# Performance work log

Measured on AMD Instinct MI355X. Metric: run time of the kernel, lower is better.

The kernel has to match this reference:

```python
import jax, jax.numpy as jnp
import numpy as np

N_POINTS = 400000
N_SEG = 4096


def setup_inputs() -> dict:
    key = jax.random.key(0)
    ks = jax.random.split(key, 8)
    inp = {
        "features": jax.random.normal(ks[0], (N_POINTS, 11), dtype=jnp.float32),
        "super_indices": jax.random.randint(ks[1], (N_POINTS,), 0, N_SEG, dtype=jnp.int64) if jax.config.jax_enable_x64 else jax.random.randint(ks[1], (N_POINTS,), 0, N_SEG).astype(jnp.int32),
        "num_segments": N_SEG,
        "W1": jax.random.normal(ks[2], (11, 128), dtype=jnp.float32) * 0.02,
        "b1": jnp.zeros((128,), jnp.float32),
        "W2": jax.random.normal(ks[3], (128, 256), dtype=jnp.float32) * 0.02,
        "b2": jnp.zeros((256,), jnp.float32),
        "W3": jax.random.normal(ks[4], (512, 512), dtype=jnp.float32) * 0.02,
        "b3": jnp.zeros((512,), jnp.float32),
        "W4": jax.random.normal(ks[5], (512, 384), dtype=jnp.float32) * 0.02,
        "b4": jnp.zeros((384,), jnp.float32),
    }
    return inp


def reference(features, super_indices, num_segments, W1, b1, W2, b2, W3, b3, W4, b4):
    # first_conv: two 1x1 Conv1d == per-point linears (no activation between, as in source)
    h = features @ W1 + b1            # [N,128]
    h = h @ W2 + b2                   # [N,256]
    # per-superpoint global max (torch.max over group points)
    g = jax.ops.segment_max(h, super_indices, num_segments=num_segments)  # [S,256]
    # concat broadcasted group-global with local features -> 512 channels
    hcat = jnp.concatenate([g[super_indices], h], axis=-1)                # [N,512]
    # second_conv: Conv1d(512,512,1) -> ReLU -> Conv1d(512,token_embed_dim,1)
    z = jax.nn.relu(hcat @ W3 + b3)   # [N,512]
    z = z @ W4 + b4                   # [N,384]
    # final per-superpoint max pool -> one token per superpoint
    sp_features = jax.ops.segment_max(z, super_indices, num_segments=num_segments)  # [S,384]
    return sp_features
```

## Files before the change

### kernel.cpp

```cpp
#include <hip/hip_runtime.h>
#include <stdint.h>

#define GAS __attribute__((address_space(1)))
#define LAS __attribute__((address_space(3)))

typedef unsigned short u16;
typedef short short8 __attribute__((ext_vector_type(8)));
typedef __bf16 bf16x8 __attribute__((ext_vector_type(8)));
typedef float floatx4 __attribute__((ext_vector_type(4)));

__device__ __forceinline__ u16 f2bf(float f) {
  uint32_t u = __builtin_bit_cast(uint32_t, f);
  u += 0x7FFFu + ((u >> 16) & 1u);
  return (u16)(u >> 16);
}
__device__ __forceinline__ float bf2f(u16 h) {
  return __builtin_bit_cast(float, (uint32_t)h << 16);
}
__device__ __forceinline__ void split_bf(float v, u16& hi, u16& lo) {
  hi = f2bf(v);
  float r = v - bf2f(hi);
  if (!(r == r)) r = 0.f;
  lo = f2bf(r);
}

__device__ __forceinline__ void atomicMaxF(float* addr, float val) {
  if (!(val > *(volatile const float*)addr)) return;
  if (val >= 0.f) atomicMax((int*)addr, __builtin_bit_cast(int, val));
  else            atomicMin((unsigned int*)addr, __builtin_bit_cast(unsigned int, val));
}

__device__ __forceinline__ void async16(const void* g, const void* lds) {
  __builtin_amdgcn_global_load_lds((GAS const uint32_t*)g, (LAS uint32_t*)lds, 16, 0, 0);
}

__device__ __forceinline__ floatx4 mfma_bf16(short8 a, short8 b, floatx4 c) {
  return __builtin_amdgcn_mfma_f32_16x16x32_bf16(
      __builtin_bit_cast(bf16x8, a), __builtin_bit_cast(bf16x8, b), c, 0, 0, 0);
}

__global__ void k_init(float* __restrict__ g, float* __restrict__ out,
                       int* __restrict__ hist, int ng, int no, int nh) {
  int i = blockIdx.x * 256 + threadIdx.x;
  if (i < ng) g[i] = -INFINITY;
  else if (i < ng + no) out[i - ng] = -INFINITY;
  else if (i < ng + no + nh) hist[i - ng - no] = 0;
}

__global__ void k_hist(const int* __restrict__ idx, int* __restrict__ hist, int n) {
  int p = blockIdx.x * 256 + threadIdx.x;
  if (p < n) atomicAdd(&hist[idx[p]], 1);
}

__global__ __launch_bounds__(1024) void k_scan(const int* __restrict__ hist,
                                               int* __restrict__ offs, int* __restrict__ cur) {
  __shared__ int buf[2][1024];
  int t = threadIdx.x;
  int local[4];
  int s = 0;
#pragma unroll
  for (int j = 0; j < 4; ++j) { local[j] = hist[t * 4 + j]; s += local[j]; }
  buf[0][t] = s;
  __syncthreads();
  int pb = 0;
  for (int d = 1; d < 1024; d <<= 1) {
    int v = buf[pb][t] + (t >= d ? buf[pb][t - d] : 0);
    buf[pb ^ 1][t] = v;
    pb ^= 1;
    __syncthreads();
  }
  int run = (t == 0) ? 0 : buf[pb][t - 1];
#pragma unroll
  for (int j = 0; j < 4; ++j) { offs[t * 4 + j] = run; cur[t * 4 + j] = run; run += local[j]; }
}

__global__ void k_scatter(const int* __restrict__ idx, int* __restrict__ cur,
                          int* __restrict__ perm, int* __restrict__ segp, int n) {
  int p = blockIdx.x * 256 + threadIdx.x;
  if (p >= n) return;
  int s = idx[p];
  int r = atomicAdd(&cur[s], 1);
  perm[r] = p;
  segp[r] = s;
}

__global__ void k_h1(const float* __restrict__ feat, const int* __restrict__ perm,
                     const float* __restrict__ W1, const float* __restrict__ b1,
                     u16* __restrict__ h1hi, u16* __restrict__ h1lo,
                     int pt_off, int npts_chunk) {
  int gid = blockIdx.x * 256 + threadIdx.x;
  int p = gid >> 7, c = gid & 127;
  if (p >= npts_chunk) return;
  int o = perm[pt_off + p];
  float v = b1[c];
#pragma unroll
  for (int j = 0; j < 11; ++j) v += feat[o * 11 + j] * W1[j * 128 + c];
  u16 hi, lo; split_bf(v, hi, lo);
  h1hi[gid] = hi; h1lo[gid] = lo;
}

__global__ void k_wprep(const float* __restrict__ W, u16* __restrict__ bt, int K, int N) {
  int gid = blockIdx.x * 256 + threadIdx.x;
  if (gid >= K * N) return;
  int c = gid / K, k = gid - c * K;
  float v = W[(size_t)k * N + c];
  u16 hi, lo; split_bf(v, hi, lo);
  size_t b = (size_t)c * (3 * K);
  bt[b + k] = hi; bt[b + K + k] = lo; bt[b + 2 * K + k] = hi;
}

__global__ void k_w23(const float* __restrict__ W2, const float* __restrict__ W3,
                      const float* __restrict__ b2, const float* __restrict__ b3,
                      float* __restrict__ W23, float* __restrict__ b23) {
  int gid = blockIdx.x * 256 + threadIdx.x;
  if (gid < 128 * 512) {
    int j = gid >> 9, c = gid & 511;
    float s = 0.f;
#pragma unroll 4
    for (int t = 0; t < 256; ++t) s += W2[j * 256 + t] * W3[(size_t)(256 + t) * 512 + c];
    W23[gid] = s;
  } else if (gid < 128 * 512 + 512) {
    int c = gid - 128 * 512;
    float s = b3[c];
    for (int t = 0; t < 256; ++t) s += b2[t] * W3[(size_t)(256 + t) * 512 + c];
    b23[c] = s;
  }
}

__global__ void k_prep3(const float* __restrict__ W3, const float* __restrict__ W23,
                        u16* __restrict__ bt) {
  int gid = blockIdx.x * 256 + threadIdx.x;
  if (gid >= 512 * 384) return;
  int c = gid / 384, k = gid - c * 384;
  float v = (k < 256) ? W3[(size_t)k * 512 + c] : W23[(size_t)(k - 256) * 512 + c];
  u16 hi, lo; split_bf(v, hi, lo);
  size_t b = (size_t)c * 1152;
  bt[b + k] = hi; bt[b + 384 + k] = lo; bt[b + 768 + k] = hi;
}

__global__ void k_gsplit(const float* __restrict__ g, u16* __restrict__ ghi,
                         u16* __restrict__ glo, int n) {
  int i = blockIdx.x * 256 + threadIdx.x;
  if (i >= n) return;
  u16 hi, lo; split_bf(g[i], hi, lo);
  ghi[i] = hi; glo[i] = lo;
}

template <int MODE, int KP, int NT, int CW>
__global__ __launch_bounds__(256) void k_gemm(
    const u16* __restrict__ a0, const u16* __restrict__ a1,
    const u16* __restrict__ a2, const u16* __restrict__ a3,
    const u16* __restrict__ bt, const float* __restrict__ bias,
    const int* __restrict__ segp, int mt0, int nb,
    float* __restrict__ gmax, u16* __restrict__ whi, u16* __restrict__ wlo) {
  __shared__ __align__(16) union {
    struct { u16 A[2][128 * 64]; u16 B[2][128 * 64]; } st;
    float ct[128 * 66];
  } sm;
  const int tid = threadIdx.x;
  const int w = tid >> 6, lane = tid & 63;

  const int work_total = nb * NT;
  const int spx = (work_total + 7) >> 3;
  const int wk = (blockIdx.x & 7) * spx + (blockIdx.x >> 3);
  if (wk >= work_total) return;
  const int mtl = wk / NT, ct = wk - mtl * NT;

  const int wr = w & 1, wc = w >> 1;
  const int l15 = lane & 15, l4 = lane >> 4;
  const int sub = lane >> 3;
  const int kc8 = (lane & 7) * 8;

  int arl[4], bcol[4], gq[4];
#pragma unroll
  for (int q = 0; q < 4; ++q) {
    int rr = (q * 4 + w) * 8 + sub;
    arl[q] = mtl * 128 + rr;
    bcol[q] = ct * 128 + rr;
    if constexpr (MODE == 1) gq[q] = segp[(mt0 + mtl) * 128 + rr];
  }

  auto stage = [&](int kt, int buf) {
    const int kbase = kt * 64 + kc8;
#pragma unroll
    for (int q = 0; q < 4; ++q) {
      const u16* src;
      if constexpr (MODE == 0) {
        int r = kbase >> 7, k = kbase & 127;
        src = ((r == 2) ? a1 : a0) + (size_t)arl[q] * 128 + k;
      } else if constexpr (MODE == 1) {
        int r = kbase / 384, inner = kbase - r * 384;
        bool lo = (r == 2);
        if (inner < 256) src = (lo ? a2 : a0) + (size_t)gq[q] * 256 + inner;
        else             src = (lo ? a3 : a1) + (size_t)arl[q] * 128 + (inner - 256);
      } else {
        int r = kbase >> 9, inner = kbase & 511;
        src = ((r == 2) ? a1 : a0) + (size_t)arl[q] * 512 + inner;
      }
      async16(src, &sm.st.A[buf][(q * 4 + w) * 512]);
    }
#pragma unroll
    for (int q = 0; q < 4; ++q)
      async16(bt + (size_t)bcol[q] * KP + kbase, &sm.st.B[buf][(q * 4 + w) * 512]);
  };

  floatx4 zero = {0.f, 0.f, 0.f, 0.f};
  floatx4 acc[4][4];
#pragma unroll
  for (int mi = 0; mi < 4; ++mi)
#pragma unroll
    for (int ni = 0; ni < 4; ++ni) acc[mi][ni] = zero;

  constexpr int NKT = KP / 64;
  stage(0, 0);
  __syncthreads();
  int cur = 0;
  for (int kt = 0; kt < NKT; ++kt) {
    if (kt + 1 < NKT) stage(kt + 1, cur ^ 1);
#pragma unroll
    for (int kk = 0; kk < 2; ++kk) {
      short8 af[4], bfr[4];
#pragma unroll
      for (int mi = 0; mi < 4; ++mi)
        af[mi] = *(const short8*)&sm.st.A[cur][(wr * 64 + mi * 16 + l15) * 64 + kk * 32 + l4 * 8];
#pragma unroll
      for (int ni = 0; ni < 4; ++ni)
        bfr[ni] = *(const short8*)&sm.st.B[cur][(wc * 64 + ni * 16 + l15) * 64 + kk * 32 + l4 * 8];
#pragma unroll
      for (int mi = 0; mi < 4; ++mi)
#pragma unroll
        for (int ni = 0; ni < 4; ++ni)
          acc[mi][ni] = mfma_bf16(af[mi], bfr[ni], acc[mi][ni]);
    }
    __syncthreads();
    cur ^= 1;
  }

  if constexpr (MODE == 1) {
#pragma unroll
    for (int ni = 0; ni < 4; ++ni) {
      const int col = ct * 128 + wc * 64 + ni * 16 + l15;
      const float bv = bias[col];
#pragma unroll
      for (int mi = 0; mi < 4; ++mi) {
        const int rl0 = mtl * 128 + wr * 64 + mi * 16 + l4 * 4;
#pragma unroll
        for (int r = 0; r < 4; ++r) {
          float v = fmaxf(acc[mi][ni][r] + bv, 0.f);
          u16 hi, lo; split_bf(v, hi, lo);
          whi[(size_t)(rl0 + r) * 512 + col] = hi;
          wlo[(size_t)(rl0 + r) * 512 + col] = lo;
        }
      }
    }
  } else {
#pragma unroll
    for (int h = 0; h < 2; ++h) {
      __syncthreads();
      if (wc == h) {
#pragma unroll
        for (int ni = 0; ni < 4; ++ni) {
          const int cl = ni * 16 + l15;
          const float bv = bias[ct * 128 + h * 64 + cl];
#pragma unroll
          for (int mi = 0; mi < 4; ++mi) {
            const int row0 = wr * 64 + mi * 16 + l4 * 4;
#pragma unroll
            for (int r = 0; r < 4; ++r)
              sm.ct[(row0 + r) * 66 + cl] = acc[mi][ni][r] + bv;
          }
        }
      }
      __syncthreads();
      if (tid < 128) {
        const int col = tid & 63, rh = tid >> 6;
        const int cg = ct * 128 + h * 64 + col;
        const int base = (mt0 + mtl) * 128 + rh * 64;
        float run = sm.ct[(rh * 64) * 66 + col];
        int curs = segp[base];
        for (int r = 1; r < 64; ++r) {
          int s = segp[base + r];
          float v = sm.ct[(rh * 64 + r) * 66 + col];
          if (s != curs) {
            atomicMaxF(&gmax[(size_t)curs * CW + cg], run);
            run = v; curs = s;
          } else {
            run = fmaxf(run, v);
          }
        }
        atomicMaxF(&gmax[(size_t)curs * CW + cg], run);
      }
    }
  }
}

static inline int swgrid(int work) { return 8 * ((work + 7) / 8); }

extern "C" void kernel_launch(void* const* d_in, const int* in_sizes, int n_in,
                              void* d_out, int out_size, void* d_ws, size_t ws_size,
                              hipStream_t stream) {
  const float* feat = (const float*)d_in[0];
  const int* sidx   = (const int*)d_in[1];
  const float* W1 = (const float*)d_in[3];
  const float* b1 = (const float*)d_in[4];
  const float* W2 = (const float*)d_in[5];
  const float* b2 = (const float*)d_in[6];
  const float* W3 = (const float*)d_in[7];
  const float* b3 = (const float*)d_in[8];
  const float* W4 = (const float*)d_in[9];
  const float* b4 = (const float*)d_in[10];
  float* out = (float*)d_out;
  (void)n_in;

  const int S  = out_size / 384;
  const int NP = in_sizes[1];
  const int MT = NP / 128;

  char* ws = (char*)d_ws;
  size_t off = 0;
  auto carve = [&](size_t bytes) -> void* {
    void* p = ws + off;
    off += (bytes + 255) & ~(size_t)255;
    return p;
  };
  float* g   = (float*)carve((size_t)S * 256 * 4);
  u16* ghi   = (u16*)carve((size_t)S * 256 * 2);
  u16* glo   = (u16*)carve((size_t)S * 256 * 2);
  u16* B2t   = (u16*)carve((size_t)256 * 384 * 2);
  u16* B3t   = (u16*)carve((size_t)512 * 1152 * 2);
  u16* B4t   = (u16*)carve((size_t)384 * 1536 * 2);
  float* W23 = (float*)carve((size_t)128 * 512 * 4);
  float* b23 = (float*)carve((size_t)512 * 4);
  int* hist  = (int*)carve((size_t)S * 4);
  int* offs  = (int*)carve((size_t)S * 4);
  int* curp  = (int*)carve((size_t)S * 4);
  int* perm  = (int*)carve((size_t)NP * 4);
  int* segp  = (int*)carve((size_t)NP * 4);

  const size_t per_block = (size_t)128 * (128 * 2 * 2 + 512 * 2 * 2) + 4 * 256;
  size_t remain = (ws_size > off + 4096) ? (ws_size - off - 4096) : 0;
  int cb = (int)(remain / per_block);
  if (cb < 1) cb = 1;
  if (cb > MT) cb = MT;
  u16* h1hi = (u16*)carve((size_t)cb * 128 * 128 * 2);
  u16* h1lo = (u16*)carve((size_t)cb * 128 * 128 * 2);
  u16* z1hi = (u16*)carve((size_t)cb * 128 * 512 * 2);
  u16* z1lo = (u16*)carve((size_t)cb * 128 * 512 * 2);

  k_init<<<(S * (256 + 384 + 1) + 255) / 256, 256, 0, stream>>>(g, out, hist,
                                                                S * 256, S * 384, S);
  k_hist<<<(NP + 255) / 256, 256, 0, stream>>>(sidx, hist, NP);
  k_scan<<<1, 1024, 0, stream>>>(hist, offs, curp);
  k_scatter<<<(NP + 255) / 256, 256, 0, stream>>>(sidx, curp, perm, segp, NP);

  k_wprep<<<(128 * 256 + 255) / 256, 256, 0, stream>>>(W2, B2t, 128, 256);
  k_w23<<<(128 * 512 + 512 + 255) / 256, 256, 0, stream>>>(W2, W3, b2, b3, W23, b23);
  k_prep3<<<(512 * 384 + 255) / 256, 256, 0, stream>>>(W3, W23, B3t);
  k_wprep<<<(512 * 384 + 255) / 256, 256, 0, stream>>>(W4, B4t, 512, 384);

  for (int done = 0; done < MT; done += cb) {
    int nb = (MT - done < cb) ? (MT - done) : cb;
    int pts = nb * 128;
    k_h1<<<(pts * 128) / 256, 256, 0, stream>>>(feat, perm, W1, b1, h1hi, h1lo,
                                                done * 128, pts);
    k_gemm<0, 384, 2, 256><<<swgrid(nb * 2), 256, 0, stream>>>(
        h1hi, h1lo, nullptr, nullptr, B2t, b2, segp, done, nb, g, nullptr, nullptr);
  }
  k_gsplit<<<(S * 256 + 255) / 256, 256, 0, stream>>>(g, ghi, glo, S * 256);

  for (int done = 0; done < MT; done += cb) {
    int nb = (MT - done < cb) ? (MT - done) : cb;
    int pts = nb * 128;
    k_h1<<<(pts * 128) / 256, 256, 0, stream>>>(feat, perm, W1, b1, h1hi, h1lo,
                                                done * 128, pts);
    k_gemm<1, 1152, 4, 0><<<swgrid(nb * 4), 256, 0, stream>>>(
        ghi, h1hi, glo, h1lo, B3t, b23, segp, done, nb, nullptr, z1hi, z1lo);
    k_gemm<2, 1536, 3, 384><<<swgrid(nb * 3), 256, 0, stream>>>(
        z1hi, z1lo, nullptr, nullptr, B4t, b4, segp, done, nb, out, nullptr, nullptr);
  }
}
```

Measured before the change: 2.637 ms.

## Widen GEMM N-tiles, halve K-step, and XOR-swizzle LDS staging

The GEMM kernel now takes a TILEN template parameter, so the N tile grows from 128 to 256 (or 192 for the final layer). Each block therefore reuses its staged A rows across more output columns and fewer blocks re-read the same A data. The K step drops from 64 to 32 so the shared-memory footprint stays bounded, and launch bounds ask for two blocks per CU. Staging uses an XOR chunk swizzle to avoid LDS bank conflicts, and the gathered segment indices are cached in shared memory. The cost is more accumulator registers per thread, twice as many K iterations with their barriers, and fewer blocks in flight.

```diff
diff --git a/kernel.cpp b/kernel.cpp
--- a/kernel.cpp
+++ b/kernel.cpp
@@ -146,17 +146,25 @@
   ghi[i] = hi; glo[i] = lo;
 }
 
-template <int MODE, int KP, int NT, int CW>
-__global__ __launch_bounds__(256) void k_gemm(
+template <int MODE, int KP, int NT, int CW, int TILEN>
+__global__ __launch_bounds__(256, 2) void k_gemm(
     const u16* __restrict__ a0, const u16* __restrict__ a1,
     const u16* __restrict__ a2, const u16* __restrict__ a3,
     const u16* __restrict__ bt, const float* __restrict__ bias,
     const int* __restrict__ segp, int mt0, int nb,
     float* __restrict__ gmax, u16* __restrict__ whi, u16* __restrict__ wlo) {
+  constexpr int WN = TILEN / 2;
+  constexpr int NI = WN / 16;
+  constexpr int NKT = KP / 32;
+  constexpr int NSLOT = 512 + TILEN * 4;
+  constexpr int NIT = NSLOT / 256;
+
   __shared__ __align__(16) union {
-    struct { u16 A[2][128 * 64]; u16 B[2][128 * 64]; } st;
+    struct { u16 A[2][4096]; u16 B[2][TILEN * 32]; } st;
     float ct[128 * 66];
   } sm;
+  __shared__ int segl[128];
+
   const int tid = threadIdx.x;
   const int w = tid >> 6, lane = tid & 63;
 
@@ -164,82 +172,86 @@
   const int spx = (work_total + 7) >> 3;
   const int wk = (blockIdx.x & 7) * spx + (blockIdx.x >> 3);
   if (wk >= work_total) return;
-  const int mtl = wk / NT, ct = wk - mtl * NT;
+  const int mtl = wk / NT, ctile = wk - mtl * NT;
 
   const int wr = w & 1, wc = w >> 1;
   const int l15 = lane & 15, l4 = lane >> 4;
-  const int sub = lane >> 3;
-  const int kc8 = (lane & 7) * 8;
-
-  int arl[4], bcol[4], gq[4];
-#pragma unroll
-  for (int q = 0; q < 4; ++q) {
-    int rr = (q * 4 + w) * 8 + sub;
-    arl[q] = mtl * 128 + rr;
-    bcol[q] = ct * 128 + rr;
-    if constexpr (MODE == 1) gq[q] = segp[(mt0 + mtl) * 128 + rr];
+  const int chsw = (l15 >> 1) & 3;
+
+  if constexpr (MODE == 1) {
+    if (tid < 128) segl[tid] = segp[(mt0 + mtl) * 128 + tid];
+    __syncthreads();
   }
 
   auto stage = [&](int kt, int buf) {
-    const int kbase = kt * 64 + kc8;
-#pragma unroll
-    for (int q = 0; q < 4; ++q) {
+    const int kt32 = kt * 32;
+#pragma unroll
+    for (int i = 0; i < NIT; ++i) {
+      const int s = tid + i * 256;
+      const int sw = (tid & ~63) + i * 256;
       const u16* src;
-      if constexpr (MODE == 0) {
-        int r = kbase >> 7, k = kbase & 127;
-        src = ((r == 2) ? a1 : a0) + (size_t)arl[q] * 128 + k;
-      } else if constexpr (MODE == 1) {
-        int r = kbase / 384, inner = kbase - r * 384;
-        bool lo = (r == 2);
-        if (inner < 256) src = (lo ? a2 : a0) + (size_t)gq[q] * 256 + inner;
-        else             src = (lo ? a3 : a1) + (size_t)arl[q] * 128 + (inner - 256);
+      if (s < 512) {
+        const int row = s >> 2, ch = s & 3;
+        const int kg = kt32 + ((ch ^ ((row >> 1) & 3)) << 3);
+        const int rl = mtl * 128 + row;
+        if constexpr (MODE == 0) {
+          int r = kg >> 7, k = kg & 127;
+          src = ((r == 2) ? a1 : a0) + (size_t)rl * 128 + k;
+        } else if constexpr (MODE == 1) {
+          int r = kg / 384, inner = kg - r * 384;
+          bool lo = (r == 2);
+          if (inner < 256) src = (lo ? a2 : a0) + (size_t)segl[row] * 256 + inner;
+          else             src = (lo ? a3 : a1) + (size_t)rl * 128 + (inner - 256);
+        } else {
+          int r = kg >> 9, inner = kg & 511;
+          src = ((r == 2) ? a1 : a0) + (size_t)rl * 512 + inner;
+        }
       } else {
-        int r = kbase >> 9, inner = kbase & 511;
-        src = ((r == 2) ? a1 : a0) + (size_t)arl[q] * 512 + inner;
+        const int sb = s - 512;
+        const int col = sb >> 2, ch = sb & 3;
+        const int kg = kt32 + ((ch ^ ((col >> 1) & 3)) << 3);
+        src = bt + (size_t)(ctile * TILEN + col) * KP + kg;
       }
-      async16(src, &sm.st.A[buf][(q * 4 + w) * 512]);
+      const void* ldsb = (sw < 512)
+          ? (const void*)&sm.st.A[buf][sw * 8]
+          : (const void*)&sm.st.B[buf][(sw - 512) * 8];
+      async16(src, ldsb);
     }
-#pragma unroll
-    for (int q = 0; q < 4; ++q)
-      async16(bt + (size_t)bcol[q] * KP + kbase, &sm.st.B[buf][(q * 4 + w) * 512]);
   };
 
   floatx4 zero = {0.f, 0.f, 0.f, 0.f};
-  floatx4 acc[4][4];
+  floatx4 acc[4][NI];
 #pragma unroll
   for (int mi = 0; mi < 4; ++mi)
 #pragma unroll
-    for (int ni = 0; ni < 4; ++ni) acc[mi][ni] = zero;
-
-  constexpr int NKT = KP / 64;
+    for (int ni = 0; ni < NI; ++ni) acc[mi][ni] = zero;
+
   stage(0, 0);
   __syncthreads();
   int cur = 0;
   for (int kt = 0; kt < NKT; ++kt) {
     if (kt + 1 < NKT) stage(kt + 1, cur ^ 1);
-#pragma unroll
-    for (int kk = 0; kk < 2; ++kk) {
-      short8 af[4], bfr[4];
-#pragma unroll
-      for (int mi = 0; mi < 4; ++mi)
-        af[mi] = *(const short8*)&sm.st.A[cur][(wr * 64 + mi * 16 + l15) * 64 + kk * 32 + l4 * 8];
-#pragma unroll
-      for (int ni = 0; ni < 4; ++ni)
-        bfr[ni] = *(const short8*)&sm.st.B[cur][(wc * 64 + ni * 16 + l15) * 64 + kk * 32 + l4 * 8];
-#pragma unroll
-      for (int mi = 0; mi < 4; ++mi)
-#pragma unroll
-        for (int ni = 0; ni < 4; ++ni)
-          acc[mi][ni] = mfma_bf16(af[mi], bfr[ni], acc[mi][ni]);
-    }
+    const int co = (l4 ^ chsw) * 8;
+    short8 af[4], bfr[NI];
+#pragma unroll
+    for (int mi = 0; mi < 4; ++mi)
+      af[mi] = *(const short8*)&sm.st.A[cur][(wr * 64 + mi * 16 + l15) * 32 + co];
+#pragma unroll
+    for (int ni = 0; ni < NI; ++ni)
+      bfr[ni] = *(const short8*)&sm.st.B[cur][(wc * WN + ni * 16 + l15) * 32 + co];
+#pragma unroll
+    for (int mi = 0; mi < 4; ++mi)
+#pragma unroll
+      for (int ni = 0; ni < NI; ++ni)
+        acc[mi][ni] = mfma_bf16(af[mi], bfr[ni], acc[mi][ni]);
     __syncthreads();
     cur ^= 1;
   }
 
   if constexpr (MODE == 1) {
 #pragma unroll
-    for (int ni = 0; ni < 4; ++ni) {
-      const int col = ct * 128 + wc * 64 + ni * 16 + l15;
+    for (int ni = 0; ni < NI; ++ni) {
+      const int col = ctile * TILEN + wc * WN + ni * 16 + l15;
       const float bv = bias[col];
 #pragma unroll
       for (int mi = 0; mi < 4; ++mi) {
@@ -254,14 +266,16 @@
       }
     }
   } else {
-#pragma unroll
-    for (int h = 0; h < 2; ++h) {
+    constexpr int NHALF = TILEN / 64;
+#pragma unroll
+    for (int h = 0; h < NHALF; ++h) {
       __syncthreads();
-      if (wc == h) {
-#pragma unroll
-        for (int ni = 0; ni < 4; ++ni) {
-          const int cl = ni * 16 + l15;
-          const float bv = bias[ct * 128 + h * 64 + cl];
+#pragma unroll
+      for (int ni = 0; ni < NI; ++ni) {
+        const int cstart = wc * WN + ni * 16;
+        if (cstart >= h * 64 && cstart < h * 64 + 64) {
+          const int cl = cstart - h * 64 + l15;
+          const float bv = bias[ctile * TILEN + h * 64 + cl];
 #pragma unroll
           for (int mi = 0; mi < 4; ++mi) {
             const int row0 = wr * 64 + mi * 16 + l4 * 4;
@@ -274,7 +288,7 @@
       __syncthreads();
       if (tid < 128) {
         const int col = tid & 63, rh = tid >> 6;
-        const int cg = ct * 128 + h * 64 + col;
+        const int cg = ctile * TILEN + h * 64 + col;
         const int base = (mt0 + mtl) * 128 + rh * 64;
         float run = sm.ct[(rh * 64) * 66 + col];
         int curs = segp[base];
@@ -363,7 +377,7 @@
     int pts = nb * 128;
     k_h1<<<(pts * 128) / 256, 256, 0, stream>>>(feat, perm, W1, b1, h1hi, h1lo,
                                                 done * 128, pts);
-    k_gemm<0, 384, 2, 256><<<swgrid(nb * 2), 256, 0, stream>>>(
+    k_gemm<0, 384, 1, 256, 256><<<swgrid(nb), 256, 0, stream>>>(
         h1hi, h1lo, nullptr, nullptr, B2t, b2, segp, done, nb, g, nullptr, nullptr);
   }
   k_gsplit<<<(S * 256 + 255) / 256, 256, 0, stream>>>(g, ghi, glo, S * 256);
@@ -373,9 +387,9 @@
     int pts = nb * 128;
     k_h1<<<(pts * 128) / 256, 256, 0, stream>>>(feat, perm, W1, b1, h1hi, h1lo,
                                                 done * 128, pts);
-    k_gemm<1, 1152, 4, 0><<<swgrid(nb * 4), 256, 0, stream>>>(
+    k_gemm<1, 1152, 2, 0, 256><<<swgrid(nb * 2), 256, 0, stream>>>(
         ghi, h1hi, glo, h1lo, B3t, b23, segp, done, nb, nullptr, z1hi, z1lo);
-    k_gemm<2, 1536, 3, 384><<<swgrid(nb * 3), 256, 0, stream>>>(
+    k_gemm<2, 1536, 2, 384, 192><<<swgrid(nb * 2), 256, 0, stream>>>(
         z1hi, z1lo, nullptr, nullptr, B4t, b4, segp, done, nb, out, nullptr, nullptr);
   }
 }
```

New measurement: 2.803 ms. 6.3% more time.
